# Optimization experiments

Measured on AMD Instinct MI355X. Metric: run time of the kernel, lower is better.

## Reference

```python
import jax, jax.numpy as jnp
import numpy as np

N_IN = 128
N_OUT = 128
K_DEG = 3
G = 8
GRID_LO, GRID_HI = 0.0, 1.0
BATCH = 512
E = N_IN * N_OUT  # number of edges


def setup_inputs() -> dict:
    key = jax.random.key(0)
    k1, k2, k3 = jax.random.split(key, 3)
    x = jax.random.uniform(k1, (BATCH, N_IN), dtype=jnp.float32)
    # Extended uniform knot vector: G+1 interior points padded by K_DEG on each side -> G+2k+1 knots.
    h = (GRID_HI - GRID_LO) / G
    knots = GRID_LO + h * jnp.arange(-K_DEG, G + K_DEG + 1, dtype=jnp.float32)  # (G+2k+1,)
    grid = jnp.tile(knots, (E, 1))  # (E, G+2k+1), one knot vector per edge
    c_basis = 0.1 * jax.random.normal(k2, (E, G + K_DEG), dtype=jnp.float32)
    c_res = (1.0 / np.sqrt(N_IN)) * jax.random.normal(k3, (N_OUT, N_IN), dtype=jnp.float32)
    c_spl = jnp.ones((N_OUT, N_IN), dtype=jnp.float32)
    return {"x": x, "grid": grid, "c_basis": c_basis, "c_res": c_res, "c_spl": c_spl}


def _basis(x, grid):
    # x: (B, n_in) -> broadcast to every edge (edge e = o*n_in + i), transposed to (E, B)
    xe = jnp.tile(x.T, (N_OUT, 1))[:, None, :]   # (E, 1, B)
    g = grid[:, :, None]                          # (E, n_knots, 1)
    # degree-0 indicator splines: (E, n_knots-1, B)
    b = ((xe >= g[:, :-1]) & (xe < g[:, 1:])).astype(x.dtype)
    # Cox-de Boor recurrence, k steps; each step shrinks the basis axis by 1
    for Kd in range(1, K_DEG + 1):
        left = (xe - g[:, :-(Kd + 1)]) / (g[:, Kd:-1] - g[:, :-(Kd + 1)])
        right = (g[:, Kd + 1:] - xe) / (g[:, Kd + 1:] - g[:, 1:-Kd])
        b = left * b[:, :-1] + right * b[:, 1:]
    return b  # (E, G+k, B)


def reference(x, grid, c_basis, c_res, c_spl):
    batch = x.shape[0]
    Bi = _basis(x, grid)                               # (E, G+k, B)
    spl = jnp.einsum('ej,ejb->eb', c_basis, Bi).T      # (B, E)
    spl = spl.reshape(batch, N_OUT, N_IN)              # edge e = o*n_in + i
    res = jnp.einsum('bi,oi->bo', jax.nn.silu(x), c_res)
    out = res + jnp.einsum('boi,oi->bo', spl, c_spl)   # (B, n_out)
    return out
```

## Files before the change

kernel.cpp:

```cpp
#include <hip/hip_runtime.h>
#include <hip/hip_bf16.h>
#include <math.h>

#define N_IN   128
#define N_OUT  128
#define BATCH  512
#define NB     11
#define FJ     12
#define KD     (N_IN * FJ)
#define LSTR   1544

typedef __attribute__((ext_vector_type(8))) short bf16x8;
typedef __attribute__((ext_vector_type(4))) float f32x4;

static __device__ __forceinline__ unsigned short bf1(float a) {
    __hip_bfloat16 h = __float2bfloat16(a);
    return *reinterpret_cast<unsigned short*>(&h);
}
static __device__ __forceinline__ unsigned pkbf(float a, float b) {
    return (unsigned)bf1(a) | ((unsigned)bf1(b) << 16);
}

__global__ __launch_bounds__(512) void kan_fused4(
    const float* __restrict__ x, const float* __restrict__ grid,
    const float* __restrict__ c_basis, const float* __restrict__ c_res,
    const float* __restrict__ c_spl, float* __restrict__ out)
{
    __shared__ unsigned short Fl[16 * LSTR];
    __shared__ unsigned short Wl[16 * LSTR];
    __shared__ float Spl[16 * N_IN];
    __shared__ float part[8][256];
    const int t   = threadIdx.x;
    const int bid = blockIdx.x;
    const int m0  = (bid >> 3) * 16;
    const int n0  = (bid & 7) * 16;

    float xr[4];
    #pragma unroll
    for (int r = 0; r < 4; ++r) {
        const int p = t + r * 512;
        xr[r] = x[(m0 + (p >> 7)) * N_IN + (p & 127)];
    }
    const float4 sp4 = ((const float4*)(c_spl + n0 * N_IN))[t];
    const float4 rs4 = ((const float4*)(c_res + n0 * N_IN))[t];
    const float* CB  = c_basis + (size_t)n0 * N_IN * NB;
    float4 cbv[11];
    #pragma unroll
    for (int m = 0; m < 11; ++m) cbv[m] = ((const float4*)CB)[m * 512 + t];

    ((float4*)Spl)[t] = sp4;

    #pragma unroll
    for (int k = 0; k < 4; ++k) {
        const int e = 4 * t + k;
        Wl[(e >> 7) * LSTR + (e & 127) * FJ + 11] = bf1(((const float*)&rs4)[k]);
    }

    const float lo = grid[3];
    const float hr = 1.0f / (grid[4] - grid[3]);
    #pragma unroll
    for (int r = 0; r < 4; ++r) {
        const int p  = t + r * 512;
        const int bl = p >> 7;
        const int i  = p & 127;
        const float xv = xr[r];
        const float s  = (xv - lo) * hr;
        int c = (int)s; c = c < 0 ? 0 : (c > 7 ? 7 : c);
        const float u  = s - (float)c;
        const float um = 1.0f - u;
        const float u2 = u * u, u3 = u2 * u;
        const float B0 = um * um * um * (1.0f / 6.0f);
        const float B1 = (3.0f * u3 - 6.0f * u2 + 4.0f) * (1.0f / 6.0f);
        const float B2 = (-3.0f * u3 + 3.0f * u2 + 3.0f * u + 1.0f) * (1.0f / 6.0f);
        const float B3 = u3 * (1.0f / 6.0f);
        float fv[12];
        #pragma unroll
        for (int j = 0; j < NB; ++j) {
            const int d = j - c;
            fv[j] = (d == 0) ? B0 : (d == 1) ? B1 : (d == 2) ? B2 : (d == 3) ? B3 : 0.0f;
        }
        fv[11] = xv / (1.0f + __expf(-xv));
        unsigned int* dst = (unsigned int*)&Fl[bl * LSTR + i * FJ];
        #pragma unroll
        for (int j = 0; j < 6; ++j)
            dst[j] = pkbf(fv[2 * j], fv[2 * j + 1]);
    }

    __syncthreads();

    #pragma unroll
    for (int m = 0; m < 11; ++m) {
        const int f0 = (m * 512 + t) * 4;
        #pragma unroll
        for (int k = 0; k < 4; ++k) {
            const int f = f0 + k;
            const int e = f / 11;
            const float w = ((const float*)&cbv[m])[k] * Spl[e];
            Wl[f + e + ((e >> 7) << 3)] = bf1(w);
        }
    }

    __syncthreads();

    const int wv   = t >> 6;
    const int lane = t & 63;
    const int row  = lane & 15;
    const int kq   = (lane >> 4) * 8;
    const int k0   = wv * (KD / 8);
    f32x4 acc = {0.f, 0.f, 0.f, 0.f};
    #pragma unroll
    for (int ks = 0; ks < 6; ++ks) {
        const int k = k0 + ks * 32 + kq;
        const bf16x8 a = *(const bf16x8*)&Fl[row * LSTR + k];
        const bf16x8 b = *(const bf16x8*)&Wl[row * LSTR + k];
        acc = __builtin_amdgcn_mfma_f32_16x16x32_bf16(a, b, acc, 0, 0, 0);
    }

    #pragma unroll
    for (int r = 0; r < 4; ++r)
        part[wv][((lane >> 4) * 4 + r) * 16 + (lane & 15)] = acc[r];
    __syncthreads();

    if (t < 256) {
        float s = part[0][t] + part[1][t] + part[2][t] + part[3][t]
                + part[4][t] + part[5][t] + part[6][t] + part[7][t];
        out[(m0 + (t >> 4)) * N_OUT + n0 + (t & 15)] = s;
    }
}

extern "C" void kernel_launch(void* const* d_in, const int* in_sizes, int n_in,
                              void* d_out, int out_size, void* d_ws, size_t ws_size,
                              hipStream_t stream) {
    const float* x       = (const float*)d_in[0];
    const float* grid    = (const float*)d_in[1];
    const float* c_basis = (const float*)d_in[2];
    const float* c_res   = (const float*)d_in[3];
    const float* c_spl   = (const float*)d_in[4];
    float* out = (float*)d_out;

    kan_fused4<<<256, 512, 0, stream>>>(x, grid, c_basis, c_res, c_spl, out);
}
```

Baseline: 12.59 us.

## Build weight tile per-edge in registers, drop Spl staging and extra barrier

Each thread now loads one edge's 11 basis coefficients, c_spl and c_res directly, scales them in registers, and writes the packed bf16 weight row to LDS with 8-byte stores. This removes the Spl shared array, the divide-by-11 scatter loop and one __syncthreads. Feature-row stores are widened to uint2 as well. The trade-off is that global loads become strided per thread (44-byte stride, scalar loads) instead of coalesced float4 loads, which may cost memory efficiency.

```diff
diff --git a/kernel.cpp b/kernel.cpp
--- a/kernel.cpp
+++ b/kernel.cpp
@@ -21,14 +21,13 @@
     return (unsigned)bf1(a) | ((unsigned)bf1(b) << 16);
 }
 
-__global__ __launch_bounds__(512) void kan_fused4(
+__global__ __launch_bounds__(512) void kan_fused5(
     const float* __restrict__ x, const float* __restrict__ grid,
     const float* __restrict__ c_basis, const float* __restrict__ c_res,
     const float* __restrict__ c_spl, float* __restrict__ out)
 {
     __shared__ unsigned short Fl[16 * LSTR];
     __shared__ unsigned short Wl[16 * LSTR];
-    __shared__ float Spl[16 * N_IN];
     __shared__ float part[8][256];
     const int t   = threadIdx.x;
     const int bid = blockIdx.x;
@@ -41,19 +40,15 @@
         const int p = t + r * 512;
         xr[r] = x[(m0 + (p >> 7)) * N_IN + (p & 127)];
     }
-    const float4 sp4 = ((const float4*)(c_spl + n0 * N_IN))[t];
-    const float4 rs4 = ((const float4*)(c_res + n0 * N_IN))[t];
-    const float* CB  = c_basis + (size_t)n0 * N_IN * NB;
-    float4 cbv[11];
+    float cb[4][NB], spl[4], res[4];
     #pragma unroll
-    for (int m = 0; m < 11; ++m) cbv[m] = ((const float4*)CB)[m * 512 + t];
-
-    ((float4*)Spl)[t] = sp4;
-
-    #pragma unroll
-    for (int k = 0; k < 4; ++k) {
-        const int e = 4 * t + k;
-        Wl[(e >> 7) * LSTR + (e & 127) * FJ + 11] = bf1(((const float*)&rs4)[k]);
+    for (int r = 0; r < 4; ++r) {
+        const size_t e = (size_t)n0 * N_IN + t + 512 * r;
+        const float* cp = c_basis + e * NB;
+        #pragma unroll
+        for (int j = 0; j < NB; ++j) cb[r][j] = cp[j];
+        spl[r] = c_spl[e];
+        res[r] = c_res[e];
     }
 
     const float lo = grid[3];
@@ -80,33 +75,33 @@
             fv[j] = (d == 0) ? B0 : (d == 1) ? B1 : (d == 2) ? B2 : (d == 3) ? B3 : 0.0f;
         }
         fv[11] = xv / (1.0f + __expf(-xv));
-        unsigned int* dst = (unsigned int*)&Fl[bl * LSTR + i * FJ];
+        uint2* dst = (uint2*)&Fl[bl * LSTR + i * FJ];
+        dst[0] = make_uint2(pkbf(fv[0], fv[1]), pkbf(fv[2],  fv[3]));
+        dst[1] = make_uint2(pkbf(fv[4], fv[5]), pkbf(fv[6],  fv[7]));
+        dst[2] = make_uint2(pkbf(fv[8], fv[9]), pkbf(fv[10], fv[11]));
+    }
+
+    #pragma unroll
+    for (int r = 0; r < 4; ++r) {
+        const int ol = (t >> 7) + 4 * r;
+        const int i  = t & 127;
+        float wv[12];
         #pragma unroll
-        for (int j = 0; j < 6; ++j)
-            dst[j] = pkbf(fv[2 * j], fv[2 * j + 1]);
+        for (int j = 0; j < NB; ++j) wv[j] = spl[r] * cb[r][j];
+        wv[11] = res[r];
+        uint2* dst = (uint2*)&Wl[ol * LSTR + i * FJ];
+        dst[0] = make_uint2(pkbf(wv[0], wv[1]), pkbf(wv[2],  wv[3]));
+        dst[1] = make_uint2(pkbf(wv[4], wv[5]), pkbf(wv[6],  wv[7]));
+        dst[2] = make_uint2(pkbf(wv[8], wv[9]), pkbf(wv[10], wv[11]));
     }
 
     __syncthreads();
 
-    #pragma unroll
-    for (int m = 0; m < 11; ++m) {
-        const int f0 = (m * 512 + t) * 4;
-        #pragma unroll
-        for (int k = 0; k < 4; ++k) {
-            const int f = f0 + k;
-            const int e = f / 11;
-            const float w = ((const float*)&cbv[m])[k] * Spl[e];
-            Wl[f + e + ((e >> 7) << 3)] = bf1(w);
-        }
-    }
-
-    __syncthreads();
-
-    const int wv   = t >> 6;
+    const int wv_  = t >> 6;
     const int lane = t & 63;
     const int row  = lane & 15;
     const int kq   = (lane >> 4) * 8;
-    const int k0   = wv * (KD / 8);
+    const int k0   = wv_ * (KD / 8);
     f32x4 acc = {0.f, 0.f, 0.f, 0.f};
     #pragma unroll
     for (int ks = 0; ks < 6; ++ks) {
@@ -118,7 +113,7 @@
 
     #pragma unroll
     for (int r = 0; r < 4; ++r)
-        part[wv][((lane >> 4) * 4 + r) * 16 + (lane & 15)] = acc[r];
+        part[wv_][((lane >> 4) * 4 + r) * 16 + (lane & 15)] = acc[r];
     __syncthreads();
 
     if (t < 256) {
@@ -138,5 +133,5 @@
     const float* c_spl   = (const float*)d_in[4];
     float* out = (float*)d_out;
 
-    kan_fused4<<<256, 512, 0, stream>>>(x, grid, c_basis, c_res, c_spl, out);
+    kan_fused5<<<256, 512, 0, stream>>>(x, grid, c_basis, c_res, c_spl, out);
 }
```

Result: faster. 11.41 us, median of 2 (-9.4%).
